# Kernel optimization log

Measured on AMD Instinct MI355X. Metric: run time of the kernel, lower is better.

## Reference

```python
import jax, jax.numpy as jnp
import numpy as np

N_NODES, N_HEDGES, N_INC = 50000, 10000, 500000
IN_VDIM, IN_EDIM = 128, 128
OUT_VDIM, OUT_EDIM, H = 64, 64, 2


def segment_softmax(scores, seg_ids, num_segments):
    # scores: [E, H, 1]; softmax over edges sharing the same seg_id
    m = jax.ops.segment_max(scores, seg_ids, num_segments=num_segments)
    m = jax.lax.stop_gradient(m)
    ex = jnp.exp(scores - m[seg_ids])
    s = jax.ops.segment_sum(ex, seg_ids, num_segments=num_segments)
    return ex / s[seg_ids]


def setup_inputs() -> dict:
    key = jax.random.key(0)
    ks = jax.random.split(key, 16)
    g = 1.414  # relu gain (xavier-ish scale folded into normal init)
    inp = {
        "vfeat": jax.random.normal(ks[0], (N_NODES, IN_VDIM), jnp.float32),
        "efeat": jax.random.normal(ks[1], (N_HEDGES, IN_EDIM), jnp.float32),
        "inc_node": jax.random.randint(ks[2], (N_INC,), 0, N_NODES),
        "inc_hedge": jax.random.randint(ks[3], (N_INC,), 0, N_HEDGES),
        # params (W stored [in, out] so x @ W == torch Linear)
        "W_ke": jax.random.normal(ks[4], (IN_VDIM, H * OUT_EDIM), jnp.float32) * (g / np.sqrt(IN_VDIM)),
        "W_qe": jax.random.normal(ks[5], (IN_EDIM, H * OUT_EDIM), jnp.float32) * (g / np.sqrt(IN_EDIM)),
        "attn_ke": jax.random.normal(ks[6], (1, H, OUT_EDIM), jnp.float32) * 0.1,
        "attn_qe": jax.random.normal(ks[7], (1, H, OUT_EDIM), jnp.float32) * 0.1,
        "bias_e": jnp.zeros((H * OUT_EDIM,), jnp.float32),
        "W_kv": jax.random.normal(ks[8], (OUT_EDIM, H * OUT_VDIM), jnp.float32) * (g / np.sqrt(OUT_EDIM)),
        "W_qv": jax.random.normal(ks[9], (IN_VDIM, H * OUT_VDIM), jnp.float32) * (g / np.sqrt(IN_VDIM)),
        "attn_kv": jax.random.normal(ks[10], (1, H, OUT_VDIM), jnp.float32) * 0.1,
        "attn_qv": jax.random.normal(ks[11], (1, H, OUT_VDIM), jnp.float32) * 0.1,
        "bias_v": jnp.zeros((H * OUT_VDIM,), jnp.float32),
    }
    return inp


def reference(vfeat, efeat, inc_node, inc_hedge, W_ke, W_qe, attn_ke, attn_qe,
              bias_e, W_kv, W_qv, attn_kv, attn_qv, bias_v):
    # ---- Phase 1: nodes -> hyperedges (g1['in']) ----
    vfeat_ke = (vfeat @ W_ke).reshape(-1, H, OUT_EDIM)          # [N, H, De]
    efeat_qe = (efeat @ W_qe).reshape(-1, H, OUT_EDIM)          # [M, H, De]
    el = jnp.sum(vfeat_ke * attn_ke, axis=-1, keepdims=True)    # [N, H, 1]
    er = jnp.sum(efeat_qe * attn_qe, axis=-1, keepdims=True)    # [M, H, 1]
    e = jax.nn.relu(el[inc_node] + er[inc_hedge])               # [E, H, 1]
    a = segment_softmax(e, inc_hedge, N_HEDGES)                 # [E, H, 1]
    msg = vfeat_ke[inc_node] * a                                # [E, H, De]
    efeat_agg = jax.ops.segment_sum(msg, inc_hedge, num_segments=N_HEDGES)
    efeat_agg = efeat_agg + bias_e.reshape(1, H, OUT_EDIM)
    efeat_out = efeat_agg.mean(axis=1)                          # [M, De]

    # ---- Phase 2: hyperedges -> nodes (g2['con']) ----
    efeat_kv = (efeat_out @ W_kv).reshape(-1, H, OUT_VDIM)      # [M, H, Dv]
    vfeat_qv = (vfeat @ W_qv).reshape(-1, H, OUT_VDIM)          # [N, H, Dv]
    el2 = jnp.sum(efeat_kv * attn_kv, axis=-1, keepdims=True)   # [M, H, 1]
    er2 = jnp.sum(vfeat_qv * attn_qv, axis=-1, keepdims=True)   # [N, H, 1]
    e2 = jax.nn.relu(el2[inc_hedge] + er2[inc_node])            # [E, H, 1]
    a2 = segment_softmax(e2, inc_node, N_NODES)                 # [E, H, 1]
    msg2 = efeat_kv[inc_hedge] * a2                             # [E, H, Dv]
    vfeat_agg = jax.ops.segment_sum(msg2, inc_node, num_segments=N_NODES)
    vfeat_agg = vfeat_agg + bias_v.reshape(1, H, OUT_VDIM)
    vfeat_out = vfeat_agg.mean(axis=1)                          # [N, Dv]

    return (vfeat_out, efeat_out)
```

## Files before the change

### kernel.cpp

```cpp
#include <hip/hip_runtime.h>
#include <hip/hip_bf16.h>

#define NN 50000
#define NM 10000
#define NE 500000
#define CAPH 128
#define CAPN 32
#define SPCAP 4096
#define NGH 79
#define NGN 98
#define CAPA 64

#define BIN_BLK   240
#define GEMM_TILES ((NN + 63) / 64)
#define ROWS_BLK  300
#define P1_GRID   (BIN_BLK + GEMM_TILES + ROWS_BLK)

typedef short bf16x8 __attribute__((ext_vector_type(8)));
typedef unsigned short u16x8 __attribute__((ext_vector_type(8)));
typedef float f32x4 __attribute__((ext_vector_type(4)));

static const size_t OFF_VKE  = 0;
static const size_t OFF_EKV  = 3200000;
static const size_t OFF_EL   = 3840000;
static const size_t OFF_ER   = 3940000;
static const size_t OFF_EL2  = 3960000;
static const size_t OFF_ER2  = 3980000;
static const size_t OFF_CQE  = 4080000;
static const size_t OFF_CQV  = 4080256;
static const size_t OFF_WT   = 4080512;
static const size_t OFF_WT2  = 4088704;
static const size_t OFF_INT  = 4093000;
static const size_t I_CUR    = 0;
static const size_t I_SPCH   = 60000;
static const size_t I_SPCN   = 60001;
static const size_t I_CSRH   = 60004;
static const size_t I_CSRN   = 700004;
static const size_t I_SPH    = 1500004;
static const size_t I_SPN    = 1508196;
static const size_t I_REGH   = 1516388;
static const size_t I_REGN   = 2729828;
static const size_t I_CNTAH  = 4235108;
static const size_t I_CNTAN  = 4254068;

__device__ __forceinline__ unsigned short f2bf(float f) {
    unsigned int u = __float_as_uint(f);
    unsigned int r = (u + 0x7fffu + ((u >> 16) & 1u)) >> 16;
    return (unsigned short)r;
}
__device__ __forceinline__ float bflo(unsigned int p) { return __uint_as_float(p << 16); }
__device__ __forceinline__ float bfhi(unsigned int p) { return __uint_as_float(p & 0xffff0000u); }

__global__ void prep_kernel(const float* __restrict__ W_qe, const float* __restrict__ attn_qe,
                            float* __restrict__ cqe,
                            const float* __restrict__ W_qv, const float* __restrict__ attn_qv,
                            float* __restrict__ cqv,
                            const float* __restrict__ W_ke, unsigned short* __restrict__ Wt,
                            const float* __restrict__ W_kv, unsigned int* __restrict__ Wt2,
                            int* __restrict__ spc_h, int* __restrict__ spc_n) {
    int b = blockIdx.x, t = threadIdx.x;
    if (b == 0 && t == 0) { *spc_h = 0; *spc_n = 0; }
    if (b < 2) {
        const float* W    = b ? W_qv : W_qe;
        const float* attn = b ? attn_qv : attn_qe;
        float*       c    = b ? cqv : cqe;
        int h = t >> 7, k = t & 127;
        float s = 0.f;
        #pragma unroll 8
        for (int j = 0; j < 64; ++j) s += W[k * 128 + h * 64 + j] * attn[h * 64 + j];
        c[h * 128 + k] = s;
    } else if (b < 66) {
        int col = (b - 2) * 2 + (t >> 7), k = t & 127;
        Wt[col * 128 + k] = f2bf(W_ke[k * 128 + col]);
    } else {
        int i = (b - 66) * 256 + t;
        int k = i >> 6, l = i & 63;
        unsigned int lo = f2bf(W_kv[k * 128 + 2 * l]);
        unsigned int hi = f2bf(W_kv[k * 128 + 2 * l + 1]);
        Wt2[k * 64 + l] = (hi << 16) | lo;
    }
}

struct P1Smem {
    unsigned short Abuf[64 * 128];
    unsigned short Wbuf[128 * 128];
};

__global__ __launch_bounds__(256) void phase1_kernel(
        const int* __restrict__ inc_n, const int* __restrict__ inc_h,
        unsigned int* __restrict__ regA_H, unsigned int* __restrict__ regA_N,
        int* __restrict__ cntA_H, int* __restrict__ cntA_N,
        int* __restrict__ spc_h, int2* __restrict__ spill_h,
        int* __restrict__ spc_n, int2* __restrict__ spill_n,
        const float* __restrict__ X, const unsigned short* __restrict__ Wt,
        const float* __restrict__ attn, const float* __restrict__ cq,
        unsigned short* __restrict__ Y, float* __restrict__ el, float* __restrict__ er2,
        const float* __restrict__ EF, const float* __restrict__ cqe,
        float* __restrict__ er) {
    __shared__ P1Smem sm;
    int bid = blockIdx.x, tid = threadIdx.x;

    if (bid < BIN_BLK) {
        int* cH = (int*)sm.Abuf;
        int* cN = cH + NGH;
        for (int i = tid; i < NGH + NGN; i += 256) cH[i] = 0;
        __syncthreads();
        int b = bid;
        for (int t = bid * 256 + tid; t < NE; t += BIN_BLK * 256) {
            int n  = __builtin_nontemporal_load(&inc_n[t]);
            int hd = __builtin_nontemporal_load(&inc_h[t]);
            unsigned int p = (unsigned int)n | ((unsigned int)hd << 16);
            int gh = hd >> 7;
            int sh = atomicAdd(&cH[gh], 1);
            if (sh < CAPA)
                regA_H[((size_t)b * NGH + gh) * CAPA + sh] = p;
            else { int s = atomicAdd(spc_h, 1); if (s < SPCAP) spill_h[s] = make_int2(hd, n); }
            int gn = n >> 9;
            int sn = atomicAdd(&cN[gn], 1);
            if (sn < CAPA)
                regA_N[((size_t)b * NGN + gn) * CAPA + sn] = p;
            else { int s = atomicAdd(spc_n, 1); if (s < SPCAP) spill_n[s] = make_int2(n, hd); }
        }
        __syncthreads();
        for (int i = tid; i < NGH; i += 256) cntA_H[b * NGH + i] = cH[i];
        for (int i = tid; i < NGN; i += 256) cntA_N[b * NGN + i] = cN[i];
        return;
    }
    if (bid >= BIN_BLK + GEMM_TILES) {
        int wave = tid >> 6, lane = tid & 63;
        for (int g = bid - BIN_BLK - GEMM_TILES; g < (NM + 3) / 4; g += ROWS_BLK) {
            int m = g * 4 + wave;
            if (m < NM) {
                float x0 = EF[(size_t)m * 128 + lane];
                float x1 = EF[(size_t)m * 128 + 64 + lane];
                float a0 = x0 * cqe[lane]       + x1 * cqe[64 + lane];
                float a1 = x0 * cqe[128 + lane] + x1 * cqe[192 + lane];
                for (int off = 32; off > 0; off >>= 1) {
                    a0 += __shfl_down(a0, off);
                    a1 += __shfl_down(a1, off);
                }
                if (lane == 0) { er[m * 2] = a0; er[m * 2 + 1] = a1; }
            }
        }
        return;
    }

    int m0 = (bid - BIN_BLK) * 64;
    const int R = NN;
    {
        const u16x8* Wg = reinterpret_cast<const u16x8*>(Wt);
        #pragma unroll
        for (int i = 0; i < 8; ++i) {
            int idx16 = i * 256 + tid;
            u16x8 w8 = Wg[idx16];
            int col = idx16 >> 4, kb = idx16 & 15;
            int us = (col * 128 + kb * 8) ^ ((col & 7) << 3);
            *reinterpret_cast<u16x8*>(&sm.Wbuf[us]) = w8;
        }
    }
    {
        int r = tid >> 2, q = tid & 3;
        int m = m0 + r;
        float p0 = 0.f, p1 = 0.f;
        if (m < R) {
            const float4* Xr = reinterpret_cast<const float4*>(X + (size_t)m * 128 + q * 32);
            #pragma unroll
            for (int i2 = 0; i2 < 4; ++i2) {
                float4 u = Xr[i2 * 2], v = Xr[i2 * 2 + 1];
                int k0 = q * 32 + i2 * 8;
                u16x8 w8;
                w8[0] = f2bf(u.x); w8[1] = f2bf(u.y); w8[2] = f2bf(u.z); w8[3] = f2bf(u.w);
                w8[4] = f2bf(v.x); w8[5] = f2bf(v.y); w8[6] = f2bf(v.z); w8[7] = f2bf(v.w);
                int us = (r * 128 + k0) ^ ((r & 7) << 3);
                *reinterpret_cast<u16x8*>(&sm.Abuf[us]) = w8;
                p0 += u.x * cq[k0] + u.y * cq[k0 + 1] + u.z * cq[k0 + 2] + u.w * cq[k0 + 3]
                    + v.x * cq[k0 + 4] + v.y * cq[k0 + 5] + v.z * cq[k0 + 6] + v.w * cq[k0 + 7];
                p1 += u.x * cq[128 + k0] + u.y * cq[128 + k0 + 1] + u.z * cq[128 + k0 + 2] + u.w * cq[128 + k0 + 3]
                    + v.x * cq[128 + k0 + 4] + v.y * cq[128 + k0 + 5] + v.z * cq[128 + k0 + 6] + v.w * cq[128 + k0 + 7];
            }
        } else {
            u16x8 z = {0, 0, 0, 0, 0, 0, 0, 0};
            #pragma unroll
            for (int i2 = 0; i2 < 4; ++i2) {
                int us = (r * 128 + q * 32 + i2 * 8) ^ ((r & 7) << 3);
                *reinterpret_cast<u16x8*>(&sm.Abuf[us]) = z;
            }
        }
        p0 += __shfl_xor(p0, 1); p0 += __shfl_xor(p0, 2);
        p1 += __shfl_xor(p1, 1); p1 += __shfl_xor(p1, 2);
        if (q == 0 && m < R)
            reinterpret_cast<float2*>(er2 + (size_t)m * 2)[0] = make_float2(p0, p1);
    }
    __syncthreads();

    int l = tid & 63, w = tid >> 6;
    int lrow = w * 16 + (l & 15);
    f32x4 acc[8];
    #pragma unroll
    for (int ct = 0; ct < 8; ++ct) acc[ct] = (f32x4){0.f, 0.f, 0.f, 0.f};
    #pragma unroll
    for (int s = 0; s < 4; ++s) {
        int aidx = (lrow * 128 + s * 32 + (l >> 4) * 8) ^ ((lrow & 7) << 3);
        bf16x8 af = *reinterpret_cast<const bf16x8*>(&sm.Abuf[aidx]);
        #pragma unroll
        for (int ct = 0; ct < 8; ++ct) {
            int col = ct * 16 + (l & 15);
            int bidx = (col * 128 + s * 32 + (l >> 4) * 8) ^ ((col & 7) << 3);
            bf16x8 bf = *reinterpret_cast<const bf16x8*>(&sm.Wbuf[bidx]);
            acc[ct] = __builtin_amdgcn_mfma_f32_16x16x32_bf16(af, bf, acc[ct], 0, 0, 0);
        }
    }

    float av[8];
    #pragma unroll
    for (int ct = 0; ct < 8; ++ct) av[ct] = attn[ct * 16 + (l & 15)];
    #pragma unroll
    for (int r = 0; r < 4; ++r) {
        int m = m0 + w * 16 + (l >> 4) * 4 + r;
        bool ok = (m < R);
        #pragma unroll
        for (int ct = 0; ct < 8; ++ct)
            if (ok) Y[(size_t)m * 128 + ct * 16 + (l & 15)] = f2bf(acc[ct][r]);
        #pragma unroll
        for (int h = 0; h < 2; ++h) {
            float p = acc[h * 4][r] * av[h * 4] + acc[h * 4 + 1][r] * av[h * 4 + 1]
                    + acc[h * 4 + 2][r] * av[h * 4 + 2] + acc[h * 4 + 3][r] * av[h * 4 + 3];
            p += __shfl_xor(p, 1); p += __shfl_xor(p, 2);
            p += __shfl_xor(p, 4); p += __shfl_xor(p, 8);
            if ((l & 15) == 0 && ok) el[(size_t)m * 2 + h] = p;
        }
    }
}

__global__ __launch_bounds__(1024) void passB_kernel(
        const unsigned int* __restrict__ regA_H, const unsigned int* __restrict__ regA_N,
        const int* __restrict__ cntA_H, const int* __restrict__ cntA_N,
        unsigned short* __restrict__ csrH, unsigned short* __restrict__ csrN,
        int* __restrict__ cur,
        int* __restrict__ spc_h, int2* __restrict__ spill_h,
        int* __restrict__ spc_n, int2* __restrict__ spill_n) {
    __shared__ int cnt[512];
    __shared__ int ca[BIN_BLK];
    int tid = threadIdx.x;
    int w = tid >> 6, lane = tid & 63;

    if (blockIdx.x < NGH) {
        int g = blockIdx.x;
        for (int i = tid; i < 128; i += 1024) cnt[i] = 0;
        for (int i = tid; i < BIN_BLK; i += 1024) ca[i] = cntA_H[i * NGH + g];
        __syncthreads();
        for (int b = w; b < BIN_BLK; b += 16) {
            int cb = ca[b]; if (cb > CAPA) cb = CAPA;
            if (lane < cb) {
                unsigned int p = regA_H[((size_t)b * NGH + g) * CAPA + lane];
                int n = p & 0xFFFF, hd = p >> 16;
                int slot = atomicAdd(&cnt[hd & 127], 1);
                if (slot < CAPH) csrH[hd * CAPH + slot] = (unsigned short)n;
                else { int s = atomicAdd(spc_h, 1); if (s < SPCAP) spill_h[s] = make_int2(hd, n); }
            }
        }
        __syncthreads();
        for (int i = tid; i < 128; i += 1024) {
            int hd = g * 128 + i;
            if (hd < NM) cur[hd] = cnt[i];
        }
    } else {
        int g = blockIdx.x - NGH;
        for (int i = tid; i < 512; i += 1024) cnt[i] = 0;
        for (int i = tid; i < BIN_BLK; i += 1024) ca[i] = cntA_N[i * NGN + g];
        __syncthreads();
        for (int b = w; b < BIN_BLK; b += 16) {
            int cb = ca[b]; if (cb > CAPA) cb = CAPA;
            if (lane < cb) {
                unsigned int p = regA_N[((size_t)b * NGN + g) * CAPA + lane];
                int n = p & 0xFFFF, hd = p >> 16;
                int slot = atomicAdd(&cnt[n & 511], 1);
                if (slot < CAPN) csrN[n * CAPN + slot] = (unsigned short)hd;
                else { int s = atomicAdd(spc_n, 1); if (s < SPCAP) spill_n[s] = make_int2(n, hd); }
            }
        }
        __syncthreads();
        for (int i = tid; i < 512; i += 1024) {
            int nd = g * 512 + i;
            if (nd < NN) cur[NM + nd] = cnt[i];
        }
    }
}

__global__ __launch_bounds__(256) void gather1_kernel(
        const int* __restrict__ cur,
        const unsigned short* __restrict__ csrH,
        const unsigned int* __restrict__ vke32,
        const float* __restrict__ el, const float* __restrict__ er,
        const float* __restrict__ bias_e,
        const int* __restrict__ spc_h, const int2* __restrict__ spill_h,
        float* __restrict__ out_e,
        const unsigned int* __restrict__ Wt2, const float* __restrict__ attn_kv,
        unsigned int* __restrict__ ekv32, float* __restrict__ el2) {
    int tid = threadIdx.x;
    int wave = tid >> 6, lane = tid & 63;
    int m = blockIdx.x * 4 + wave;
    int h = lane >> 5;
    int c = cur[m]; if (c > CAPH) c = CAPH;
    int beg = m * CAPH, end = beg + c;
    float erv = er[m * 2 + h];
    float acc0 = 0.f, acc1 = 0.f, den = 0.f;
    int i = beg;
    for (; i + 7 < end; i += 8) {
        int vs[8]; unsigned int p[8]; float ex[8];
        #pragma unroll
        for (int j = 0; j < 8; ++j) vs[j] = csrH[i + j];
        #pragma unroll
        for (int j = 0; j < 8; ++j) p[j] = vke32[(size_t)vs[j] * 64 + lane];
        #pragma unroll
        for (int j = 0; j < 8; ++j) ex[j] = __expf(fmaxf(el[vs[j] * 2 + h] + erv, 0.f));
        #pragma unroll
        for (int j = 0; j < 8; ++j) {
            den += ex[j];
            acc0 += ex[j] * bflo(p[j]);
            acc1 += ex[j] * bfhi(p[j]);
        }
    }
    for (; i < end; ++i) {
        int vs = csrH[i];
        unsigned int p = vke32[(size_t)vs * 64 + lane];
        float ex = __expf(fmaxf(el[vs * 2 + h] + erv, 0.f));
        den += ex;
        acc0 += ex * bflo(p);
        acc1 += ex * bfhi(p);
    }
    int sc = *spc_h; if (sc > SPCAP) sc = SPCAP;
    for (int s = 0; s < sc; ++s) {
        int2 pr = spill_h[s];
        if (pr.x == m) {
            int vs = pr.y;
            unsigned int p = vke32[(size_t)vs * 64 + lane];
            float ex = __expf(fmaxf(el[vs * 2 + h] + erv, 0.f));
            den += ex;
            acc0 += ex * bflo(p);
            acc1 += ex * bfhi(p);
        }
    }
    float inv = (den > 0.f) ? 1.f / den : 0.f;
    acc0 *= inv; acc1 *= inv;
    float b0 = __shfl_down(acc0, 32);
    float b1 = __shfl_down(acc1, 32);
    int e0 = 2 * (lane & 31), e1 = e0 + 1;
    float o0 = 0.5f * (acc0 + b0 + bias_e[e0] + bias_e[64 + e0]);
    float o1 = 0.5f * (acc1 + b1 + bias_e[e1] + bias_e[64 + e1]);
    if (lane < 32)
        reinterpret_cast<float2*>(out_e + (size_t)m * 64)[lane] = make_float2(o0, o1);

    float g0 = 0.f, g1 = 0.f;
    #pragma unroll
    for (int k = 0; k < 64; ++k) {
        float rk = __shfl((k & 1) ? o1 : o0, k >> 1);
        unsigned int wv = Wt2[k * 64 + lane];
        g0 += rk * bflo(wv);
        g1 += rk * bfhi(wv);
    }
    ekv32[(size_t)m * 64 + lane] = ((unsigned int)f2bf(g1) << 16) | (unsigned int)f2bf(g0);
    float p = g0 * attn_kv[2 * lane] + g1 * attn_kv[2 * lane + 1];
    p += __shfl_xor(p, 1); p += __shfl_xor(p, 2); p += __shfl_xor(p, 4);
    p += __shfl_xor(p, 8); p += __shfl_xor(p, 16);
    if ((lane & 31) == 0) el2[m * 2 + (lane >> 5)] = p;
}

template<int CAP>
__global__ void gather_kernel(const int* __restrict__ cnt, const unsigned short* __restrict__ csr,
                              const unsigned int* __restrict__ src32,
                              const float* __restrict__ el_src,
                              const float* __restrict__ er_dst,
                              const float* __restrict__ bias,
                              const int* __restrict__ spc, const int2* __restrict__ spill,
                              float* __restrict__ out, int R) {
    int wave = threadIdx.x >> 6, lane = threadIdx.x & 63;
    int m = blockIdx.x * 4 + wave;
    if (m >= R) return;
    int h = lane >> 5;
    int c = cnt[m]; if (c > CAP) c = CAP;
    int beg = m * CAP, end = beg + c;
    float er = er_dst[m * 2 + h];
    float acc0 = 0.f, acc1 = 0.f, den = 0.f;
    int i = beg;
    for (; i + 7 < end; i += 8) {
        int vs[8]; unsigned int p[8]; float ex[8];
        #pragma unroll
        for (int j = 0; j < 8; ++j) vs[j] = csr[i + j];
        #pragma unroll
        for (int j = 0; j < 8; ++j) p[j] = src32[(size_t)vs[j] * 64 + lane];
        #pragma unroll
        for (int j = 0; j < 8; ++j) ex[j] = __expf(fmaxf(el_src[vs[j] * 2 + h] + er, 0.f));
        #pragma unroll
        for (int j = 0; j < 8; ++j) {
            den += ex[j];
            acc0 += ex[j] * bflo(p[j]);
            acc1 += ex[j] * bfhi(p[j]);
        }
    }
    for (; i < end; ++i) {
        int vs = csr[i];
        unsigned int p = src32[(size_t)vs * 64 + lane];
        float ex = __expf(fmaxf(el_src[vs * 2 + h] + er, 0.f));
        den += ex;
        acc0 += ex * bflo(p);
        acc1 += ex * bfhi(p);
    }
    int sc = *spc; if (sc > SPCAP) sc = SPCAP;
    for (int s = 0; s < sc; ++s) {
        int2 pr = spill[s];
        if (pr.x == m) {
            int vs = pr.y;
            unsigned int p = src32[(size_t)vs * 64 + lane];
            float ex = __expf(fmaxf(el_src[vs * 2 + h] + er, 0.f));
            den += ex;
            acc0 += ex * bflo(p);
            acc1 += ex * bfhi(p);
        }
    }
    float inv = (den > 0.f) ? 1.f / den : 0.f;
    acc0 *= inv; acc1 *= inv;
    float b0 = __shfl_down(acc0, 32);
    float b1 = __shfl_down(acc1, 32);
    if (lane < 32) {
        int e0 = 2 * lane, e1 = 2 * lane + 1;
        float o0 = 0.5f * (acc0 + b0 + bias[e0] + bias[64 + e0]);
        float o1 = 0.5f * (acc1 + b1 + bias[e1] + bias[64 + e1]);
        reinterpret_cast<float2*>(out + (size_t)m * 64)[lane] = make_float2(o0, o1);
    }
}

extern "C" void kernel_launch(void* const* d_in, const int* in_sizes, int n_in,
                              void* d_out, int out_size, void* d_ws, size_t ws_size,
                              hipStream_t stream) {
    const float* vfeat   = (const float*)d_in[0];
    const float* efeat   = (const float*)d_in[1];
    const int*   inc_n   = (const int*)d_in[2];
    const int*   inc_h   = (const int*)d_in[3];
    const float* W_ke    = (const float*)d_in[4];
    const float* W_qe    = (const float*)d_in[5];
    const float* attn_ke = (const float*)d_in[6];
    const float* attn_qe = (const float*)d_in[7];
    const float* bias_e  = (const float*)d_in[8];
    const float* W_kv    = (const float*)d_in[9];
    const float* W_qv    = (const float*)d_in[10];
    const float* attn_kv = (const float*)d_in[11];
    const float* attn_qv = (const float*)d_in[12];
    const float* bias_v  = (const float*)d_in[13];

    float* ws = (float*)d_ws;
    unsigned int*   vke = (unsigned int*)(ws + OFF_VKE);
    unsigned int*   ekv = (unsigned int*)(ws + OFF_EKV);
    float* el   = ws + OFF_EL;
    float* er   = ws + OFF_ER;
    float* el2  = ws + OFF_EL2;
    float* er2  = ws + OFF_ER2;
    float* cqe  = ws + OFF_CQE;
    float* cqv  = ws + OFF_CQV;
    unsigned short* Wt  = (unsigned short*)(ws + OFF_WT);
    unsigned int*   Wt2 = (unsigned int*)(ws + OFF_WT2);
    int*   ib      = (int*)(ws + OFF_INT);
    int*   cur     = ib + I_CUR;
    int*   spc_h   = ib + I_SPCH;
    int*   spc_n   = ib + I_SPCN;
    unsigned short* csrH = (unsigned short*)(ib + I_CSRH);
    unsigned short* csrN = (unsigned short*)(ib + I_CSRN);
    int2*  spill_h = (int2*)(ib + I_SPH);
    int2*  spill_n = (int2*)(ib + I_SPN);
    unsigned int* regA_H = (unsigned int*)(ib + I_REGH);
    unsigned int* regA_N = (unsigned int*)(ib + I_REGN);
    int*   cntA_H  = ib + I_CNTAH;
    int*   cntA_N  = ib + I_CNTAN;

    float* out_v = (float*)d_out;
    float* out_e = (float*)d_out + (size_t)NN * 64;

    prep_kernel<<<dim3(82), dim3(256), 0, stream>>>(W_qe, attn_qe, cqe, W_qv, attn_qv, cqv,
                                                    W_ke, Wt, W_kv, Wt2, spc_h, spc_n);

    phase1_kernel<<<dim3(P1_GRID), dim3(256), 0, stream>>>(
        inc_n, inc_h, regA_H, regA_N, cntA_H, cntA_N,
        spc_h, spill_h, spc_n, spill_n,
        vfeat, Wt, attn_ke, cqv, (unsigned short*)vke, el, er2,
        efeat, cqe, er);

    passB_kernel<<<dim3(NGH + NGN), dim3(1024), 0, stream>>>(
        regA_H, regA_N, cntA_H, cntA_N, csrH, csrN, cur,
        spc_h, spill_h, spc_n, spill_n);

    gather1_kernel<<<dim3(NM / 4), dim3(256), 0, stream>>>(
        cur, csrH, vke, el, er, bias_e, spc_h, spill_h, out_e,
        Wt2, attn_kv, ekv, el2);

    gather_kernel<CAPN><<<dim3((NN + 3) / 4), dim3(256), 0, stream>>>(
        cur + NM, csrN, ekv, el2, er2, bias_v, spc_n, spill_n, out_v, NN);
}
```

Measured before the change: 101.5 us.

## Overlap node-side CSR build with hyperedge gather and move Wt2 packing into passB

Splits the combined CSR-building kernel so that only the hyperedge bucketing runs before gather1, and runs the node-side bucketing as extra blocks inside the gather1 launch. The W_kv bf16 packing moves from prep into the hyperedge pass. gather1 now uses 1024-thread blocks with 16 waves each. The aim is to shorten the critical path by running independent node-bucketing work concurrently with the phase-1 gather. The cost is heterogeneous blocks sharing one launch, and the larger blocks may change occupancy.

```diff
diff --git a/kernel.cpp b/kernel.cpp
--- a/kernel.cpp
+++ b/kernel.cpp
@@ -15,6 +15,12 @@
 #define GEMM_TILES ((NN + 63) / 64)
 #define ROWS_BLK  300
 #define P1_GRID   (BIN_BLK + GEMM_TILES + ROWS_BLK)
+
+#define WT2_BLKS  4
+#define PBH_GRID  (NGH + WT2_BLKS)
+
+#define G1_BLKS   (NM / 16)
+#define G1_GRID   (G1_BLKS + NGN)
 
 typedef short bf16x8 __attribute__((ext_vector_type(8)));
 typedef unsigned short u16x8 __attribute__((ext_vector_type(8)));
@@ -56,7 +62,6 @@
                             const float* __restrict__ W_qv, const float* __restrict__ attn_qv,
                             float* __restrict__ cqv,
                             const float* __restrict__ W_ke, unsigned short* __restrict__ Wt,
-                            const float* __restrict__ W_kv, unsigned int* __restrict__ Wt2,
                             int* __restrict__ spc_h, int* __restrict__ spc_n) {
     int b = blockIdx.x, t = threadIdx.x;
     if (b == 0 && t == 0) { *spc_h = 0; *spc_n = 0; }
@@ -69,15 +74,9 @@
         #pragma unroll 8
         for (int j = 0; j < 64; ++j) s += W[k * 128 + h * 64 + j] * attn[h * 64 + j];
         c[h * 128 + k] = s;
-    } else if (b < 66) {
+    } else {
         int col = (b - 2) * 2 + (t >> 7), k = t & 127;
         Wt[col * 128 + k] = f2bf(W_ke[k * 128 + col]);
-    } else {
-        int i = (b - 66) * 256 + t;
-        int k = i >> 6, l = i & 63;
-        unsigned int lo = f2bf(W_kv[k * 128 + 2 * l]);
-        unsigned int hi = f2bf(W_kv[k * 128 + 2 * l + 1]);
-        Wt2[k * 64 + l] = (hi << 16) | lo;
     }
 }
 
@@ -232,44 +231,70 @@
     }
 }
 
-__global__ __launch_bounds__(1024) void passB_kernel(
-        const unsigned int* __restrict__ regA_H, const unsigned int* __restrict__ regA_N,
-        const int* __restrict__ cntA_H, const int* __restrict__ cntA_N,
-        unsigned short* __restrict__ csrH, unsigned short* __restrict__ csrN,
-        int* __restrict__ cur,
+__global__ __launch_bounds__(1024) void passBH_kernel(
+        const unsigned int* __restrict__ regA_H, const int* __restrict__ cntA_H,
+        unsigned short* __restrict__ csrH, int* __restrict__ cur,
         int* __restrict__ spc_h, int2* __restrict__ spill_h,
+        const float* __restrict__ W_kv, unsigned int* __restrict__ Wt2) {
+    __shared__ int cnt[128];
+    __shared__ int ca[BIN_BLK];
+    int tid = threadIdx.x;
+    if (blockIdx.x >= NGH) {
+        int i = (blockIdx.x - NGH) * 1024 + tid;
+        if (i < 4096) {
+            int k = i >> 6, l = i & 63;
+            unsigned int lo = f2bf(W_kv[k * 128 + 2 * l]);
+            unsigned int hi = f2bf(W_kv[k * 128 + 2 * l + 1]);
+            Wt2[k * 64 + l] = (hi << 16) | lo;
+        }
+        return;
+    }
+    int g = blockIdx.x;
+    int w = tid >> 6, lane = tid & 63;
+    for (int i = tid; i < 128; i += 1024) cnt[i] = 0;
+    for (int i = tid; i < BIN_BLK; i += 1024) ca[i] = cntA_H[i * NGH + g];
+    __syncthreads();
+    for (int b = w; b < BIN_BLK; b += 16) {
+        int cb = ca[b]; if (cb > CAPA) cb = CAPA;
+        if (lane < cb) {
+            unsigned int p = regA_H[((size_t)b * NGH + g) * CAPA + lane];
+            int n = p & 0xFFFF, hd = p >> 16;
+            int slot = atomicAdd(&cnt[hd & 127], 1);
+            if (slot < CAPH) csrH[hd * CAPH + slot] = (unsigned short)n;
+            else { int s = atomicAdd(spc_h, 1); if (s < SPCAP) spill_h[s] = make_int2(hd, n); }
+        }
+    }
+    __syncthreads();
+    for (int i = tid; i < 128; i += 1024) {
+        int hd = g * 128 + i;
+        if (hd < NM) cur[hd] = cnt[i];
+    }
+}
+
+__global__ __launch_bounds__(1024) void gather1_kernel(
+        const int* __restrict__ cur,
+        const unsigned short* __restrict__ csrH,
+        const unsigned int* __restrict__ vke32,
+        const float* __restrict__ el, const float* __restrict__ er,
+        const float* __restrict__ bias_e,
+        const int* __restrict__ spc_h, const int2* __restrict__ spill_h,
+        float* __restrict__ out_e,
+        const unsigned int* __restrict__ Wt2, const float* __restrict__ attn_kv,
+        unsigned int* __restrict__ ekv32, float* __restrict__ el2,
+        const unsigned int* __restrict__ regA_N, const int* __restrict__ cntA_N,
+        unsigned short* __restrict__ csrN, int* __restrict__ curN,
         int* __restrict__ spc_n, int2* __restrict__ spill_n) {
     __shared__ int cnt[512];
     __shared__ int ca[BIN_BLK];
     int tid = threadIdx.x;
-    int w = tid >> 6, lane = tid & 63;
-
-    if (blockIdx.x < NGH) {
-        int g = blockIdx.x;
-        for (int i = tid; i < 128; i += 1024) cnt[i] = 0;
-        for (int i = tid; i < BIN_BLK; i += 1024) ca[i] = cntA_H[i * NGH + g];
-        __syncthreads();
-        for (int b = w; b < BIN_BLK; b += 16) {
-            int cb = ca[b]; if (cb > CAPA) cb = CAPA;
-            if (lane < cb) {
-                unsigned int p = regA_H[((size_t)b * NGH + g) * CAPA + lane];
-                int n = p & 0xFFFF, hd = p >> 16;
-                int slot = atomicAdd(&cnt[hd & 127], 1);
-                if (slot < CAPH) csrH[hd * CAPH + slot] = (unsigned short)n;
-                else { int s = atomicAdd(spc_h, 1); if (s < SPCAP) spill_h[s] = make_int2(hd, n); }
-            }
-        }
-        __syncthreads();
-        for (int i = tid; i < 128; i += 1024) {
-            int hd = g * 128 + i;
-            if (hd < NM) cur[hd] = cnt[i];
-        }
-    } else {
-        int g = blockIdx.x - NGH;
+    int wave = tid >> 6, lane = tid & 63;
+
+    if (blockIdx.x >= G1_BLKS) {
+        int g = blockIdx.x - G1_BLKS;
         for (int i = tid; i < 512; i += 1024) cnt[i] = 0;
         for (int i = tid; i < BIN_BLK; i += 1024) ca[i] = cntA_N[i * NGN + g];
         __syncthreads();
-        for (int b = w; b < BIN_BLK; b += 16) {
+        for (int b = wave; b < BIN_BLK; b += 16) {
             int cb = ca[b]; if (cb > CAPA) cb = CAPA;
             if (lane < cb) {
                 unsigned int p = regA_N[((size_t)b * NGN + g) * CAPA + lane];
@@ -282,24 +307,12 @@
         __syncthreads();
         for (int i = tid; i < 512; i += 1024) {
             int nd = g * 512 + i;
-            if (nd < NN) cur[NM + nd] = cnt[i];
-        }
-    }
-}
-
-__global__ __launch_bounds__(256) void gather1_kernel(
-        const int* __restrict__ cur,
-        const unsigned short* __restrict__ csrH,
-        const unsigned int* __restrict__ vke32,
-        const float* __restrict__ el, const float* __restrict__ er,
-        const float* __restrict__ bias_e,
-        const int* __restrict__ spc_h, const int2* __restrict__ spill_h,
-        float* __restrict__ out_e,
-        const unsigned int* __restrict__ Wt2, const float* __restrict__ attn_kv,
-        unsigned int* __restrict__ ekv32, float* __restrict__ el2) {
-    int tid = threadIdx.x;
-    int wave = tid >> 6, lane = tid & 63;
-    int m = blockIdx.x * 4 + wave;
+            if (nd < NN) curN[nd] = cnt[i];
+        }
+        return;
+    }
+
+    int m = blockIdx.x * 16 + wave;
     int h = lane >> 5;
     int c = cur[m]; if (c > CAPH) c = CAPH;
     int beg = m * CAPH, end = beg + c;
@@ -475,8 +488,8 @@
     float* out_v = (float*)d_out;
     float* out_e = (float*)d_out + (size_t)NN * 64;
 
-    prep_kernel<<<dim3(82), dim3(256), 0, stream>>>(W_qe, attn_qe, cqe, W_qv, attn_qv, cqv,
-                                                    W_ke, Wt, W_kv, Wt2, spc_h, spc_n);
+    prep_kernel<<<dim3(66), dim3(256), 0, stream>>>(W_qe, attn_qe, cqe, W_qv, attn_qv, cqv,
+                                                    W_ke, Wt, spc_h, spc_n);
 
     phase1_kernel<<<dim3(P1_GRID), dim3(256), 0, stream>>>(
         inc_n, inc_h, regA_H, regA_N, cntA_H, cntA_N,
@@ -484,13 +497,13 @@
         vfeat, Wt, attn_ke, cqv, (unsigned short*)vke, el, er2,
         efeat, cqe, er);
 
-    passB_kernel<<<dim3(NGH + NGN), dim3(1024), 0, stream>>>(
-        regA_H, regA_N, cntA_H, cntA_N, csrH, csrN, cur,
-        spc_h, spill_h, spc_n, spill_n);
-
-    gather1_kernel<<<dim3(NM / 4), dim3(256), 0, stream>>>(
+    passBH_kernel<<<dim3(PBH_GRID), dim3(1024), 0, stream>>>(
+        regA_H, cntA_H, csrH, cur, spc_h, spill_h, W_kv, Wt2);
+
+    gather1_kernel<<<dim3(G1_GRID), dim3(1024), 0, stream>>>(
         cur, csrH, vke, el, er, bias_e, spc_h, spill_h, out_e,
-        Wt2, attn_kv, ekv, el2);
+        Wt2, attn_kv, ekv, el2,
+        regA_N, cntA_N, csrN, cur + NM, spc_n, spill_n);
 
     gather_kernel<CAPN><<<dim3((NN + 3) / 4), dim3(256), 0, stream>>>(
         cur + NM, csrN, ekv, el2, er2, bias_v, spc_n, spill_n, out_v, NN);
```

Result: slower. 103.5 us (+2.0%).
